# Kernel optimization log

Hardware: AMD Instinct MI355X
Metric: run time of the kernel (lower is better)

Reference implementation:

```python
import jax, jax.numpy as jnp
import numpy as np

HEADS = 8
DIM_HEAD = 64
SCALE = DIM_HEAD ** -0.5


def setup_inputs() -> dict:
    key = jax.random.key(0)
    k1, k2, k3 = jax.random.split(key, 3)
    b, c, n = 8, 512, 2048
    hidden = HEADS * DIM_HEAD  # 512
    x = jax.random.normal(k1, (b, c, n), dtype=jnp.float32)
    # Conv1d with kernel_size=1 == per-position linear; store weight as [out, in]
    w_qkv = jax.random.normal(k2, (3 * hidden, c), dtype=jnp.float32) * 0.02
    w_out = jax.random.normal(k3, (c, hidden), dtype=jnp.float32) * 0.02
    b_out = jnp.zeros((c,), dtype=jnp.float32)
    return {"x": x, "w_qkv": w_qkv, "w_out": w_out, "b_out": b_out}


def reference(x, w_qkv, w_out, b_out):
    b, c, n = x.shape
    h, d = HEADS, DIM_HEAD
    # to_qkv: 1x1 conv -> channel matmul; qkv: [b, 3*h*d, n]
    qkv = jnp.einsum('oc,bcn->bon', w_qkv, x)
    q, k, v = jnp.split(qkv, 3, axis=1)
    # rearrange 'b (h c) n -> b h c n'
    q = q.reshape(b, h, d, n) * SCALE
    k = k.reshape(b, h, d, n)
    v = v.reshape(b, h, d, n)
    sim = jnp.einsum('bhdi,bhdj->bhij', q, k)        # [b, h, n, n]
    attn = jax.nn.softmax(sim, axis=-1)
    out = jnp.einsum('bhij,bhdj->bhid', attn, v)     # [b, h, n, d]
    # rearrange 'b h n d -> b (h d) n'
    out = out.transpose(0, 1, 3, 2).reshape(b, h * d, n)
    # to_out: 1x1 conv with bias
    y = jnp.einsum('oc,bcn->bon', w_out, out) + b_out[None, :, None]
    return y
```

## Files before the change

### kernel.cpp

```cpp
#include <hip/hip_runtime.h>
#include <cstdint>

#define B_    8
#define NCTX  2048
#define CIN   512
#define DHEAD 64
#define HID   512
#define O3    1536

typedef __bf16 bf16x8 __attribute__((ext_vector_type(8)));
typedef short  s16x4  __attribute__((ext_vector_type(4)));
typedef float  f32x4  __attribute__((ext_vector_type(4)));

__device__ inline unsigned short f2bf(float f) {
  unsigned u = __float_as_uint(f);
  u += 0x7fffu + ((u >> 16) & 1u);
  return (unsigned short)(u >> 16);
}

__device__ inline unsigned pack_bf16(float a, float b) {
  const unsigned ua = __float_as_uint(a) + 0x8000u;
  const unsigned ub = __float_as_uint(b) + 0x8000u;
  return __builtin_amdgcn_perm(ub, ua, 0x07060302u);
}

__device__ inline void gload_lds16(const void* g, void* l) {
  __builtin_amdgcn_global_load_lds((const __attribute__((address_space(1))) unsigned int*)g,
                                   (__attribute__((address_space(3))) unsigned int*)l,
                                   16, 0, 0);
}

__device__ inline int swidx128(int row, int col) {
  return row * 128 + ((((col >> 3) ^ (row & 7))) << 3) + (col & 7);
}

__global__ __launch_bounds__(256) void k_transpose_x(const float* __restrict__ x,
                                                     unsigned short* __restrict__ xT) {
  __shared__ unsigned short tile[64][66];
  const int b  = blockIdx.z;
  const int t0 = blockIdx.x * 64;
  const int c0 = blockIdx.y * 64;
  const int tid = threadIdx.x;
  const int jj = (tid & 15) * 4;
  const int i0 = tid >> 4;
  const float* xb = x + ((size_t)b * CIN + c0) * NCTX + t0;
  #pragma unroll
  for (int s = 0; s < 4; ++s) {
    const int i = i0 + s * 16;
    const float4 v = *(const float4*)(xb + (size_t)i * NCTX + jj);
    tile[jj + 0][i] = f2bf(v.x);
    tile[jj + 1][i] = f2bf(v.y);
    tile[jj + 2][i] = f2bf(v.z);
    tile[jj + 3][i] = f2bf(v.w);
  }
  __syncthreads();
  const int ii = (tid & 15) * 4;
  const int j0 = tid >> 4;
  unsigned short* out = xT + ((size_t)b * NCTX + t0) * CIN + c0;
  #pragma unroll
  for (int s = 0; s < 4; ++s) {
    const int j = j0 + s * 16;
    ushort4 o;
    o.x = tile[j][ii + 0]; o.y = tile[j][ii + 1];
    o.z = tile[j][ii + 2]; o.w = tile[j][ii + 3];
    *(ushort4*)(out + (size_t)j * CIN + ii) = o;
  }
}

__global__ __launch_bounds__(256) void k_cvt_w(const float* __restrict__ wq,
                                               const float* __restrict__ wo,
                                               unsigned short* __restrict__ wq_bf,
                                               unsigned short* __restrict__ wo_bf) {
  const int i = (blockIdx.x * 256 + threadIdx.x) * 4;
  if (i < O3 * CIN) {
    const float4 v = *(const float4*)(wq + i);
    ushort4 o;
    o.x = f2bf(v.x); o.y = f2bf(v.y); o.z = f2bf(v.z); o.w = f2bf(v.w);
    *(ushort4*)(wq_bf + i) = o;
  } else {
    const int j = i - O3 * CIN;
    const float4 v = *(const float4*)(wo + j);
    ushort4 o;
    o.x = f2bf(v.x); o.y = f2bf(v.y); o.z = f2bf(v.z); o.w = f2bf(v.w);
    *(ushort4*)(wo_bf + j) = o;
  }
}

__global__ __launch_bounds__(256) void k_qkv(const unsigned short* __restrict__ xT,
                                             const unsigned short* __restrict__ wq,
                                             unsigned short* __restrict__ Qt,
                                             unsigned short* __restrict__ Kt,
                                             unsigned short* __restrict__ Vt) {
  __shared__ unsigned short As[128 * 64];
  __shared__ unsigned short Bs[128 * 64];
  const int b = blockIdx.z;
  const int tid = threadIdx.x;
  const int w = tid >> 6, L = tid & 63;
  const int m0 = (w & 1) * 64, n0 = (w >> 1) * 64;
  const unsigned short* Abase = xT + ((size_t)b * NCTX + blockIdx.x * 128) * CIN;
  const unsigned short* Bbase = wq + (size_t)blockIdx.y * 128 * CIN;

  f32x4 acc[4][4];
  #pragma unroll
  for (int i = 0; i < 4; ++i)
    #pragma unroll
    for (int j = 0; j < 4; ++j) acc[i][j] = f32x4{0.f, 0.f, 0.f, 0.f};

  const int sr = L >> 3;
  const int pc = L & 7;

  for (int k0 = 0; k0 < CIN; k0 += 64) {
    __syncthreads();
    #pragma unroll
    for (int s = 0; s < 4; ++s) {
      const int r0 = s * 32 + w * 8;
      const int row = r0 + sr;
      const int cc = pc ^ (row & 7);
      gload_lds16(Abase + (size_t)row * CIN + k0 + cc * 8, &As[r0 * 64]);
      gload_lds16(Bbase + (size_t)row * CIN + k0 + cc * 8, &Bs[r0 * 64]);
    }
    __syncthreads();
    #pragma unroll
    for (int kc = 0; kc < 2; ++kc) {
      const int ccf = kc * 4 + (L >> 4);
      bf16x8 af[4], bfr[4];
      #pragma unroll
      for (int mt = 0; mt < 4; ++mt) {
        const int m = m0 + mt * 16 + (L & 15);
        af[mt] = *(const bf16x8*)&As[m * 64 + ((ccf ^ (m & 7)) * 8)];
      }
      #pragma unroll
      for (int nt = 0; nt < 4; ++nt) {
        const int n = n0 + nt * 16 + (L & 15);
        bfr[nt] = *(const bf16x8*)&Bs[n * 64 + ((ccf ^ (n & 7)) * 8)];
      }
      #pragma unroll
      for (int mt = 0; mt < 4; ++mt)
        #pragma unroll
        for (int nt = 0; nt < 4; ++nt)
          acc[mt][nt] = __builtin_amdgcn_mfma_f32_16x16x32_bf16(af[mt], bfr[nt], acc[mt][nt], 0, 0, 0);
    }
  }

  const float QS = 0.125f * 1.4426950408889634f;
  #pragma unroll
  for (int mt = 0; mt < 4; ++mt) {
    #pragma unroll
    for (int nt = 0; nt < 4; ++nt) {
      const int o = blockIdx.y * 128 + n0 + nt * 16 + (L & 15);
      const int which = o >> 9;
      const int h = (o >> 6) & 7;
      const int d = o & 63;
      unsigned short* base = (which == 0) ? Qt : ((which == 1) ? Kt : Vt);
      unsigned short* dst = base + (((size_t)b * 8 + h) * NCTX) * 64 + d;
      const float scale = (which == 0) ? QS : 1.0f;
      #pragma unroll
      for (int r = 0; r < 4; ++r) {
        const int t = blockIdx.x * 128 + m0 + mt * 16 + (L >> 4) * 4 + r;
        dst[(size_t)t * 64] = f2bf(acc[mt][nt][r] * scale);
      }
    }
  }
}

__global__ __launch_bounds__(256) void k_attn(const unsigned short* __restrict__ Qt,
                                              const unsigned short* __restrict__ Kt,
                                              const unsigned short* __restrict__ Vt,
                                              unsigned short* __restrict__ AO) {
  __shared__ unsigned short Ks[128 * 64];
  __shared__ unsigned short Vs[64 * 128];
  const int bh = blockIdx.y;
  const int q0 = blockIdx.x * 128;
  const int tid = threadIdx.x;
  const int w = tid >> 6, L = tid & 63;
  const int g = L >> 4, lm = L & 15;
  const unsigned short* Qb = Qt + (size_t)bh * NCTX * 64;
  const unsigned short* Kb = Kt + (size_t)bh * NCTX * 64;
  const unsigned short* Vb = Vt + (size_t)bh * NCTX * 64;

  bf16x8 qf[2][2];
  #pragma unroll
  for (int it = 0; it < 2; ++it)
    #pragma unroll
    for (int kc = 0; kc < 2; ++kc) {
      const int row = q0 + w * 32 + it * 16 + lm;
      qf[it][kc] = *(const bf16x8*)(Qb + (size_t)row * 64 + kc * 32 + g * 8);
    }

  f32x4 oacc[4][2];
  #pragma unroll
  for (int dt = 0; dt < 4; ++dt)
    #pragma unroll
    for (int it = 0; it < 2; ++it) oacc[dt][it] = f32x4{0.f, 0.f, 0.f, 0.f};
  float m_st[2] = {-1e30f, -1e30f}, l_st[2] = {0.f, 0.f};

  const int sr = L >> 3, pc = L & 7;

  for (int jt = 0; jt < 16; ++jt) {
    const int j0 = jt * 128;
    __syncthreads();
    #pragma unroll
    for (int s = 0; s < 4; ++s) {
      const int r0 = s * 32 + w * 8;
      const int row = r0 + sr;
      gload_lds16(Kb + (size_t)(j0 + row) * 64 + ((pc ^ (row & 7)) * 8), &Ks[r0 * 64]);
    }
    #pragma unroll
    for (int s = 0; s < 4; ++s) {
      const int j = L + 64 * (s & 1);
      const int pcv = w + 4 * (s >> 1);
      const uint4 raw = *(const uint4*)(Vb + (size_t)(j0 + j) * 64 + pcv * 8);
      const unsigned vals[4] = {raw.x, raw.y, raw.z, raw.w};
      #pragma unroll
      for (int e2 = 0; e2 < 4; ++e2) {
        const int dv0 = pcv * 8 + e2 * 2;
        Vs[swidx128(dv0, j)]     = (unsigned short)(vals[e2] & 0xffffu);
        Vs[swidx128(dv0 + 1, j)] = (unsigned short)(vals[e2] >> 16);
      }
    }
    __syncthreads();

    f32x4 sacc[8][2];
    #pragma unroll
    for (int jj = 0; jj < 8; ++jj) {
      const int n = jj * 16 + lm;
      const bf16x8 kf0 = *(const bf16x8*)&Ks[n * 64 + ((g ^ (n & 7)) << 3)];
      const bf16x8 kf1 = *(const bf16x8*)&Ks[n * 64 + (((4 + g) ^ (n & 7)) << 3)];
      #pragma unroll
      for (int it = 0; it < 2; ++it) {
        f32x4 z = f32x4{0.f, 0.f, 0.f, 0.f};
        z = __builtin_amdgcn_mfma_f32_16x16x32_bf16(kf0, qf[it][0], z, 0, 0, 0);
        sacc[jj][it] = __builtin_amdgcn_mfma_f32_16x16x32_bf16(kf1, qf[it][1], z, 0, 0, 0);
      }
    }

    s16x4 pf[8][2];
    #pragma unroll
    for (int it = 0; it < 2; ++it) {
      float rm = sacc[0][it][0];
      #pragma unroll
      for (int jj = 0; jj < 8; ++jj)
        #pragma unroll
        for (int r = 0; r < 4; ++r) rm = fmaxf(rm, sacc[jj][it][r]);
      rm = fmaxf(rm, __shfl_xor(rm, 16, 64));
      rm = fmaxf(rm, __shfl_xor(rm, 32, 64));
      const float mn = fmaxf(m_st[it], rm);
      const float alpha = __builtin_amdgcn_exp2f(m_st[it] - mn);
      m_st[it] = mn;
      float rsum = 0.f;
      #pragma unroll
      for (int jj = 0; jj < 8; ++jj) {
        float p[4];
        #pragma unroll
        for (int r = 0; r < 4; ++r) {
          p[r] = __builtin_amdgcn_exp2f(sacc[jj][it][r] - mn);
          rsum += p[r];
        }
        unsigned u32x2_v[2];
        u32x2_v[0] = pack_bf16(p[0], p[1]);
        u32x2_v[1] = pack_bf16(p[2], p[3]);
        pf[jj][it] = __builtin_bit_cast(s16x4, *(const uint2*)u32x2_v);
      }
      rsum += __shfl_xor(rsum, 16, 64);
      rsum += __shfl_xor(rsum, 32, 64);
      l_st[it] = l_st[it] * alpha + rsum;
      #pragma unroll
      for (int dt = 0; dt < 4; ++dt) {
        oacc[dt][it][0] *= alpha; oacc[dt][it][1] *= alpha;
        oacc[dt][it][2] *= alpha; oacc[dt][it][3] *= alpha;
      }
    }

    #pragma unroll
    for (int jj = 0; jj < 8; ++jj) {
      #pragma unroll
      for (int dt = 0; dt < 4; ++dt) {
        const int d = dt * 16 + lm;
        const int addr = d * 128 + ((((jj * 2) + (g >> 1)) ^ (d & 7)) << 3) + ((g & 1) << 2);
        const s16x4 af = *(const s16x4*)&Vs[addr];
        #pragma unroll
        for (int it = 0; it < 2; ++it)
          oacc[dt][it] = __builtin_amdgcn_mfma_f32_16x16x16bf16_1k(af, pf[jj][it], oacc[dt][it], 0, 0, 0);
      }
    }
  }

  const int b = bh >> 3, h = bh & 7;
  #pragma unroll
  for (int it = 0; it < 2; ++it) {
    const float inv = 1.0f / l_st[it];
    const int t = q0 + w * 32 + it * 16 + lm;
    #pragma unroll
    for (int dt = 0; dt < 4; ++dt) {
      uint2 o;
      o.x = pack_bf16(oacc[dt][it][0] * inv, oacc[dt][it][1] * inv);
      o.y = pack_bf16(oacc[dt][it][2] * inv, oacc[dt][it][3] * inv);
      *(uint2*)&AO[((size_t)b * NCTX + t) * HID + h * 64 + dt * 16 + g * 4] = o;
    }
  }
}

__global__ __launch_bounds__(256) void k_proj(const unsigned short* __restrict__ wo,
                                              const unsigned short* __restrict__ AO,
                                              const float* __restrict__ bias,
                                              float* __restrict__ y) {
  __shared__ unsigned short As[128 * 64];
  __shared__ unsigned short Bs[128 * 64];
  const int b = blockIdx.z;
  const int tid = threadIdx.x;
  const int w = tid >> 6, L = tid & 63;
  const int m0 = (w & 1) * 64, n0 = (w >> 1) * 64;
  const unsigned short* Abase = wo + (size_t)blockIdx.x * 128 * HID;
  const unsigned short* Bbase = AO + ((size_t)b * NCTX + blockIdx.y * 128) * HID;

  f32x4 acc[4][4];
  #pragma unroll
  for (int i = 0; i < 4; ++i)
    #pragma unroll
    for (int j = 0; j < 4; ++j) acc[i][j] = f32x4{0.f, 0.f, 0.f, 0.f};

  const int sr = L >> 3;
  const int pc = L & 7;
  for (int k0 = 0; k0 < HID; k0 += 64) {
    __syncthreads();
    #pragma unroll
    for (int s = 0; s < 4; ++s) {
      const int r0 = s * 32 + w * 8;
      const int row = r0 + sr;
      const int cc = pc ^ (row & 7);
      gload_lds16(Abase + (size_t)row * HID + k0 + cc * 8, &As[r0 * 64]);
      gload_lds16(Bbase + (size_t)row * HID + k0 + cc * 8, &Bs[r0 * 64]);
    }
    __syncthreads();
    #pragma unroll
    for (int kc = 0; kc < 2; ++kc) {
      const int ccf = kc * 4 + (L >> 4);
      bf16x8 af[4], bfr[4];
      #pragma unroll
      for (int mt = 0; mt < 4; ++mt) {
        const int m = m0 + mt * 16 + (L & 15);
        af[mt] = *(const bf16x8*)&As[m * 64 + ((ccf ^ (m & 7)) * 8)];
      }
      #pragma unroll
      for (int nt = 0; nt < 4; ++nt) {
        const int n = n0 + nt * 16 + (L & 15);
        bfr[nt] = *(const bf16x8*)&Bs[n * 64 + ((ccf ^ (n & 7)) * 8)];
      }
      #pragma unroll
      for (int mt = 0; mt < 4; ++mt)
        #pragma unroll
        for (int nt = 0; nt < 4; ++nt)
          acc[mt][nt] = __builtin_amdgcn_mfma_f32_16x16x32_bf16(af[mt], bfr[nt], acc[mt][nt], 0, 0, 0);
    }
  }

  #pragma unroll
  for (int mt = 0; mt < 4; ++mt) {
    #pragma unroll
    for (int nt = 0; nt < 4; ++nt) {
      const int t = blockIdx.y * 128 + n0 + nt * 16 + (L & 15);
      #pragma unroll
      for (int r = 0; r < 4; ++r) {
        const int o = blockIdx.x * 128 + m0 + mt * 16 + (L >> 4) * 4 + r;
        y[((size_t)b * CIN + o) * NCTX + t] = acc[mt][nt][r] + bias[o];
      }
    }
  }
}

extern "C" void kernel_launch(void* const* d_in, const int* in_sizes, int n_in,
                              void* d_out, int out_size, void* d_ws, size_t ws_size,
                              hipStream_t stream) {
  const float* x     = (const float*)d_in[0];
  const float* w_qkv = (const float*)d_in[1];
  const float* w_out = (const float*)d_in[2];
  const float* b_out = (const float*)d_in[3];
  float* y = (float*)d_out;

  char* ws = (char*)d_ws;
  const size_t SEG = (size_t)16 * 1024 * 1024;
  unsigned short* xT    = (unsigned short*)(ws + 0 * SEG);
  unsigned short* Qt    = (unsigned short*)(ws + 1 * SEG);
  unsigned short* Kt    = (unsigned short*)(ws + 2 * SEG);
  unsigned short* Vt    = (unsigned short*)(ws + 3 * SEG);
  unsigned short* AO    = (unsigned short*)(ws + 4 * SEG);
  unsigned short* wq_bf = (unsigned short*)(ws + 5 * SEG);
  unsigned short* wo_bf = (unsigned short*)(ws + 5 * SEG + (size_t)O3 * CIN * 2);

  k_transpose_x<<<dim3(32, 8, 8), 256, 0, stream>>>(x, xT);
  k_cvt_w<<<dim3(1024), 256, 0, stream>>>(w_qkv, w_out, wq_bf, wo_bf);
  k_qkv<<<dim3(16, 12, 8), 256, 0, stream>>>(xT, wq_bf, Qt, Kt, Vt);
  k_attn<<<dim3(16, 64), 256, 0, stream>>>(Qt, Kt, Vt, AO);
  k_proj<<<dim3(4, 16, 8), 256, 0, stream>>>(wo_bf, AO, b_out, y);
}
```

Measured before the change: 274.1 us.

## Store V pre-transposed and swizzled so attention loads it via direct-to-LDS

The QKV projection now writes V in a d-major layout whose token order is permuted to match the MFMA operand order. The attention kernel can then fill its V tile with 16-byte global-to-LDS loads instead of scalar transposing LDS stores, and read V fragments as 128-bit LDS loads. The output projection swaps its A/B operands so each lane stores float4 runs along the token dimension. Softmax max and sum reductions are also vectorized. The cost is a more intricate index mapping that must stay consistent between kernels, plus strided scattered 8-byte writes of V.

Result: no change. 275.3 us (+0.5%).

```diff
diff --git a/kernel.cpp b/kernel.cpp
--- a/kernel.cpp
+++ b/kernel.cpp
@@ -11,6 +11,8 @@
 typedef __bf16 bf16x8 __attribute__((ext_vector_type(8)));
 typedef short  s16x4  __attribute__((ext_vector_type(4)));
 typedef float  f32x4  __attribute__((ext_vector_type(4)));
+typedef unsigned u32x2v __attribute__((ext_vector_type(2)));
+typedef unsigned u32x4v __attribute__((ext_vector_type(4)));
 
 __device__ inline unsigned short f2bf(float f) {
   unsigned u = __float_as_uint(f);
@@ -28,10 +30,6 @@
   __builtin_amdgcn_global_load_lds((const __attribute__((address_space(1))) unsigned int*)g,
                                    (__attribute__((address_space(3))) unsigned int*)l,
                                    16, 0, 0);
-}
-
-__device__ inline int swidx128(int row, int col) {
-  return row * 128 + ((((col >> 3) ^ (row & 7))) << 3) + (col & 7);
 }
 
 __global__ __launch_bounds__(256) void k_transpose_x(const float* __restrict__ x,
@@ -145,19 +143,28 @@
   const float QS = 0.125f * 1.4426950408889634f;
   #pragma unroll
   for (int mt = 0; mt < 4; ++mt) {
+    const int tb = blockIdx.x * 128 + m0 + mt * 16 + (L >> 4) * 4;
     #pragma unroll
     for (int nt = 0; nt < 4; ++nt) {
       const int o = blockIdx.y * 128 + n0 + nt * 16 + (L & 15);
       const int which = o >> 9;
       const int h = (o >> 6) & 7;
       const int d = o & 63;
-      unsigned short* base = (which == 0) ? Qt : ((which == 1) ? Kt : Vt);
-      unsigned short* dst = base + (((size_t)b * 8 + h) * NCTX) * 64 + d;
-      const float scale = (which == 0) ? QS : 1.0f;
-      #pragma unroll
-      for (int r = 0; r < 4; ++r) {
-        const int t = blockIdx.x * 128 + m0 + mt * 16 + (L >> 4) * 4 + r;
-        dst[(size_t)t * 64] = f2bf(acc[mt][nt][r] * scale);
+      if (which == 2) {
+        const int jt2 = tb >> 7, w2 = tb & 127;
+        const int pos = jt2 * 128 + ((w2 >> 2) & 3) * 32 + (w2 >> 4) * 4;
+        unsigned short* dst = Vt + (((size_t)b * 8 + h) * 64 + d) * 2048 + pos;
+        uint2 st;
+        st.x = pack_bf16(acc[mt][nt][0], acc[mt][nt][1]);
+        st.y = pack_bf16(acc[mt][nt][2], acc[mt][nt][3]);
+        *(uint2*)dst = st;
+      } else {
+        unsigned short* base = (which == 0) ? Qt : Kt;
+        const float scale = (which == 0) ? QS : 1.0f;
+        unsigned short* dst = base + (((size_t)b * 8 + h) * NCTX) * 64 + d;
+        #pragma unroll
+        for (int r = 0; r < 4; ++r)
+          dst[(size_t)(tb + r) * 64] = f2bf(acc[mt][nt][r] * scale);
       }
     }
   }
@@ -195,6 +202,9 @@
   float m_st[2] = {-1e30f, -1e30f}, l_st[2] = {0.f, 0.f};
 
   const int sr = L >> 3, pc = L & 7;
+  const int vr = L >> 4, vp = L & 15;
+  const int kb0 = (g ^ (lm & 7)) << 3;
+  const int kb1 = ((4 + g) ^ (lm & 7)) << 3;
 
   for (int jt = 0; jt < 16; ++jt) {
     const int j0 = jt * 128;
@@ -207,16 +217,9 @@
     }
     #pragma unroll
     for (int s = 0; s < 4; ++s) {
-      const int j = L + 64 * (s & 1);
-      const int pcv = w + 4 * (s >> 1);
-      const uint4 raw = *(const uint4*)(Vb + (size_t)(j0 + j) * 64 + pcv * 8);
-      const unsigned vals[4] = {raw.x, raw.y, raw.z, raw.w};
-      #pragma unroll
-      for (int e2 = 0; e2 < 4; ++e2) {
-        const int dv0 = pcv * 8 + e2 * 2;
-        Vs[swidx128(dv0, j)]     = (unsigned short)(vals[e2] & 0xffffu);
-        Vs[swidx128(dv0 + 1, j)] = (unsigned short)(vals[e2] >> 16);
-      }
+      const int d0 = s * 16 + w * 4;
+      const int d = d0 + vr;
+      gload_lds16(Vb + (size_t)d * 2048 + j0 + ((vp ^ (d & 15)) * 8), &Vs[d0 * 128]);
     }
     __syncthreads();
 
@@ -224,8 +227,8 @@
     #pragma unroll
     for (int jj = 0; jj < 8; ++jj) {
       const int n = jj * 16 + lm;
-      const bf16x8 kf0 = *(const bf16x8*)&Ks[n * 64 + ((g ^ (n & 7)) << 3)];
-      const bf16x8 kf1 = *(const bf16x8*)&Ks[n * 64 + (((4 + g) ^ (n & 7)) << 3)];
+      const bf16x8 kf0 = *(const bf16x8*)&Ks[n * 64 + kb0];
+      const bf16x8 kf1 = *(const bf16x8*)&Ks[n * 64 + kb1];
       #pragma unroll
       for (int it = 0; it < 2; ++it) {
         f32x4 z = f32x4{0.f, 0.f, 0.f, 0.f};
@@ -237,50 +240,53 @@
     s16x4 pf[8][2];
     #pragma unroll
     for (int it = 0; it < 2; ++it) {
-      float rm = sacc[0][it][0];
-      #pragma unroll
-      for (int jj = 0; jj < 8; ++jj)
-        #pragma unroll
-        for (int r = 0; r < 4; ++r) rm = fmaxf(rm, sacc[jj][it][r]);
+      f32x4 rm4 = __builtin_elementwise_max(sacc[0][it], sacc[1][it]);
+      #pragma unroll
+      for (int jj = 2; jj < 8; ++jj) rm4 = __builtin_elementwise_max(rm4, sacc[jj][it]);
+      float rm = fmaxf(fmaxf(rm4[0], rm4[1]), fmaxf(rm4[2], rm4[3]));
       rm = fmaxf(rm, __shfl_xor(rm, 16, 64));
       rm = fmaxf(rm, __shfl_xor(rm, 32, 64));
       const float mn = fmaxf(m_st[it], rm);
       const float alpha = __builtin_amdgcn_exp2f(m_st[it] - mn);
       m_st[it] = mn;
-      float rsum = 0.f;
+      f32x4 rsum4 = {0.f, 0.f, 0.f, 0.f};
       #pragma unroll
       for (int jj = 0; jj < 8; ++jj) {
-        float p[4];
-        #pragma unroll
-        for (int r = 0; r < 4; ++r) {
-          p[r] = __builtin_amdgcn_exp2f(sacc[jj][it][r] - mn);
-          rsum += p[r];
-        }
+        f32x4 e = sacc[jj][it];
+        e[0] = __builtin_amdgcn_exp2f(e[0] - mn);
+        e[1] = __builtin_amdgcn_exp2f(e[1] - mn);
+        e[2] = __builtin_amdgcn_exp2f(e[2] - mn);
+        e[3] = __builtin_amdgcn_exp2f(e[3] - mn);
+        rsum4 += e;
         unsigned u32x2_v[2];
-        u32x2_v[0] = pack_bf16(p[0], p[1]);
-        u32x2_v[1] = pack_bf16(p[2], p[3]);
+        u32x2_v[0] = pack_bf16(e[0], e[1]);
+        u32x2_v[1] = pack_bf16(e[2], e[3]);
         pf[jj][it] = __builtin_bit_cast(s16x4, *(const uint2*)u32x2_v);
       }
+      float rsum = (rsum4[0] + rsum4[1]) + (rsum4[2] + rsum4[3]);
       rsum += __shfl_xor(rsum, 16, 64);
       rsum += __shfl_xor(rsum, 32, 64);
       l_st[it] = l_st[it] * alpha + rsum;
       #pragma unroll
-      for (int dt = 0; dt < 4; ++dt) {
-        oacc[dt][it][0] *= alpha; oacc[dt][it][1] *= alpha;
-        oacc[dt][it][2] *= alpha; oacc[dt][it][3] *= alpha;
-      }
-    }
-
-    #pragma unroll
-    for (int jj = 0; jj < 8; ++jj) {
-      #pragma unroll
-      for (int dt = 0; dt < 4; ++dt) {
-        const int d = dt * 16 + lm;
-        const int addr = d * 128 + ((((jj * 2) + (g >> 1)) ^ (d & 7)) << 3) + ((g & 1) << 2);
-        const s16x4 af = *(const s16x4*)&Vs[addr];
+      for (int dt = 0; dt < 4; ++dt) oacc[dt][it] *= alpha;
+    }
+
+    #pragma unroll
+    for (int dt = 0; dt < 4; ++dt) {
+      const int d = dt * 16 + lm;
+      #pragma unroll
+      for (int e = 0; e < 4; ++e) {
+        const int phys = (g * 4 + e) ^ (d & 15);
+        const u32x4v vv = *(const u32x4v*)&Vs[d * 128 + phys * 8];
+        const u32x2v lo = {vv.x, vv.y};
+        const u32x2v hi = {vv.z, vv.w};
+        const s16x4 v0 = __builtin_bit_cast(s16x4, lo);
+        const s16x4 v1 = __builtin_bit_cast(s16x4, hi);
         #pragma unroll
-        for (int it = 0; it < 2; ++it)
-          oacc[dt][it] = __builtin_amdgcn_mfma_f32_16x16x16bf16_1k(af, pf[jj][it], oacc[dt][it], 0, 0, 0);
+        for (int it = 0; it < 2; ++it) {
+          oacc[dt][it] = __builtin_amdgcn_mfma_f32_16x16x16bf16_1k(v0, pf[2 * e][it], oacc[dt][it], 0, 0, 0);
+          oacc[dt][it] = __builtin_amdgcn_mfma_f32_16x16x16bf16_1k(v1, pf[2 * e + 1][it], oacc[dt][it], 0, 0, 0);
+        }
       }
     }
   }
@@ -310,8 +316,8 @@
   const int tid = threadIdx.x;
   const int w = tid >> 6, L = tid & 63;
   const int m0 = (w & 1) * 64, n0 = (w >> 1) * 64;
-  const unsigned short* Abase = wo + (size_t)blockIdx.x * 128 * HID;
-  const unsigned short* Bbase = AO + ((size_t)b * NCTX + blockIdx.y * 128) * HID;
+  const unsigned short* Abase = AO + ((size_t)b * NCTX + blockIdx.y * 128) * HID;
+  const unsigned short* Bbase = wo + (size_t)blockIdx.x * 128 * HID;
 
   f32x4 acc[4][4];
   #pragma unroll
@@ -356,14 +362,17 @@
 
   #pragma unroll
   for (int mt = 0; mt < 4; ++mt) {
+    const int t = blockIdx.y * 128 + m0 + mt * 16 + (L >> 4) * 4;
     #pragma unroll
     for (int nt = 0; nt < 4; ++nt) {
-      const int t = blockIdx.y * 128 + n0 + nt * 16 + (L & 15);
-      #pragma unroll
-      for (int r = 0; r < 4; ++r) {
-        const int o = blockIdx.x * 128 + m0 + mt * 16 + (L >> 4) * 4 + r;
-        y[((size_t)b * CIN + o) * NCTX + t] = acc[mt][nt][r] + bias[o];
-      }
+      const int o = blockIdx.x * 128 + n0 + nt * 16 + (L & 15);
+      const float bv = bias[o];
+      float4 st;
+      st.x = acc[mt][nt][0] + bv;
+      st.y = acc[mt][nt][1] + bv;
+      st.z = acc[mt][nt][2] + bv;
+      st.w = acc[mt][nt][3] + bv;
+      *(float4*)&y[((size_t)b * CIN + o) * NCTX + t] = st;
     }
   }
 }
```
